# Kernel optimization log

Measured on AMD Instinct MI355X. Metric: run time of the kernel, lower is better.

Reference implementation:

```python
import jax, jax.numpy as jnp
import numpy as np

BATCH, NODES, CH_IN, CH_OUT, N_EXPERTS = 8, 8192, 128, 128, 64

def setup_inputs() -> dict:
    key = jax.random.key(0)
    kx, kw, ks = jax.random.split(key, 3)
    x = jax.random.normal(kx, (BATCH, NODES, CH_IN), dtype=jnp.float32)
    # std = fan_in**-0.5 per self_init
    W = jax.random.normal(kw, (N_EXPERTS, CH_OUT, CH_IN), dtype=jnp.float32) * (CH_IN ** -0.5)
    sel = jax.random.randint(ks, (NODES,), 0, N_EXPERTS, dtype=jnp.int64)
    return {"x": x, "sel": sel, "W": W}

def reference(x, sel, W):
    # x: (b, n, j), W[sel]: (n, i, j) -> out: (b, n, i)
    Wsel = W[sel]  # gather a (ch_out, ch_in) matrix per node
    return jnp.einsum('bnj,nij->bni', x, Wsel)
```

## Files before the change

### kernel.cpp

```cpp
#include <hip/hip_runtime.h>

#define BATCH   8
#define NODES   8192
#define CH      128
#define NEXP    64
#define TN      16
#define MAXP    (NODES + NEXP * TN)
#define NTILES  (MAXP / TN)

typedef __attribute__((ext_vector_type(8))) short bf16x8;
typedef __attribute__((ext_vector_type(4))) float f32x4;

__device__ __forceinline__ bf16x8 cvt8(f32x4 lo, f32x4 hi) {
    bf16x8 r;
    #pragma unroll
    for (int i = 0; i < 4; ++i) {
        r[i]     = (short)__builtin_bit_cast(unsigned short, static_cast<__bf16>(lo[i]));
        r[i + 4] = (short)__builtin_bit_cast(unsigned short, static_cast<__bf16>(hi[i]));
    }
    return r;
}

__global__ __launch_bounds__(256)
void prep_kernel(const int* __restrict__ sel, const float* __restrict__ W,
                 short* __restrict__ Wbf, int* __restrict__ sorted)
{
    const int t = threadIdx.x;

    {
        const size_t base = (size_t)blockIdx.x * (CH * CH / 4);
        const float* ws = W   + base;
        short*       wd = Wbf + base;
        #pragma unroll
        for (int i = 0; i < 2; ++i) {
            int idx = (i * 256 + t) * 8;
            f32x4 lo = *reinterpret_cast<const f32x4*>(ws + idx);
            f32x4 hi = *reinterpret_cast<const f32x4*>(ws + idx + 4);
            *reinterpret_cast<bf16x8*>(wd + idx) = cvt8(lo, hi);
        }
    }

    const int e = blockIdx.x;
    if (e >= NEXP) return;

    const int wv = t >> 6;
    __shared__ int wcnt[4][NEXP];
    __shared__ int s_off, s_cnt, s_total, cursor;
    if (t < NEXP) { wcnt[0][t] = 0; wcnt[1][t] = 0; wcnt[2][t] = 0; wcnt[3][t] = 0; }
    if (t == 0) cursor = 0;
    __syncthreads();

    int myv[NODES / 256];
    #pragma unroll
    for (int i = 0; i < NODES / 256; ++i) {
        myv[i] = sel[i * 256 + t];
        atomicAdd(&wcnt[wv][myv[i]], 1);
    }
    __syncthreads();

    if (t < NEXP) {
        int c = wcnt[0][t] + wcnt[1][t] + wcnt[2][t] + wcnt[3][t];
        int p = (c + TN - 1) & ~(TN - 1);
        int scan = p;
        #pragma unroll
        for (int d = 1; d < NEXP; d <<= 1) {
            int v = __shfl_up(scan, d);
            if (t >= d) scan += v;
        }
        if (t == e)        { s_off = scan - p; s_cnt = c; }
        if (t == NEXP - 1) s_total = scan;
    }
    __syncthreads();

    const int off = s_off, myc = s_cnt;
    const int pad = (myc + TN - 1) & ~(TN - 1);

    for (int i = myc + t; i < pad; i += 256) sorted[off + i] = -1;

    if (e == NEXP - 1) {
        for (int i = s_total + t; i < MAXP; i += 256) sorted[i] = -1;
    }

    #pragma unroll
    for (int i = 0; i < NODES / 256; ++i) {
        if (myv[i] == e) {
            int pos = atomicAdd(&cursor, 1);
            sorted[off + pos] = i * 256 + t;
        }
    }
}

__global__ __launch_bounds__(512)
void gemm_kernel(const float* __restrict__ x, const int* __restrict__ sel,
                 const short* __restrict__ Wbf, float* __restrict__ out,
                 const int* __restrict__ sorted)
{
    __shared__ int s_nodes[TN];
    __shared__ int s_expert;

    const int tid  = threadIdx.x;
    const int tile = blockIdx.x;

    if (tid < TN) s_nodes[tid] = sorted[tile * TN + tid];
    if (tid == 0) {
        int n0 = sorted[tile * TN];
        s_expert = (n0 >= 0) ? sel[n0] : -1;
    }
    __syncthreads();

    const int e = s_expert;
    if (e < 0) return;

    const int wave = tid >> 6;
    const int lane = tid & 63;
    const int m16  = lane & 15;
    const int quad = lane >> 4;

    const int r    = wave * 16 + m16;
    const int node = s_nodes[r >> 3];
    const int b    = r & 7;
    const int nd   = (node >= 0) ? node : 0;
    const float* xrow  = x + ((size_t)(b * NODES + nd)) * CH;
    const short* wbase = Wbf + (size_t)e * CH * CH;

    f32x4 acc[8];
    #pragma unroll
    for (int ct = 0; ct < 8; ++ct) acc[ct] = (f32x4){0.f, 0.f, 0.f, 0.f};

    #pragma unroll
    for (int kk = 0; kk < 4; ++kk) {
        const int k0 = kk * 32 + quad * 8;

        f32x4 lo = *reinterpret_cast<const f32x4*>(xrow + k0);
        f32x4 hi = *reinterpret_cast<const f32x4*>(xrow + k0 + 4);
        bf16x8 afrag = cvt8(lo, hi);

        #pragma unroll
        for (int ct = 0; ct < 8; ++ct) {
            bf16x8 bfrag = *reinterpret_cast<const bf16x8*>(
                wbase + (size_t)(ct * 16 + m16) * CH + k0);
            acc[ct] = __builtin_amdgcn_mfma_f32_16x16x32_bf16(
                          afrag, bfrag, acc[ct], 0, 0, 0);
        }
    }

    #pragma unroll
    for (int reg = 0; reg < 4; ++reg) {
        int rr = wave * 16 + quad * 4 + reg;
        int nn = s_nodes[rr >> 3];
        if (nn < 0) continue;
        int bb = rr & 7;
        float* orow = out + ((size_t)(bb * NODES + nn)) * CH;
        #pragma unroll
        for (int ct = 0; ct < 8; ++ct)
            orow[ct * 16 + m16] = acc[ct][reg];
    }
}

extern "C" void kernel_launch(void* const* d_in, const int* in_sizes, int n_in,
                              void* d_out, int out_size, void* d_ws, size_t ws_size,
                              hipStream_t stream)
{
    const float* x   = (const float*)d_in[0];
    const int*   sel = (const int*)  d_in[1];
    const float* W   = (const float*)d_in[2];
    float*       out = (float*)d_out;

    short* Wbf    = (short*)d_ws;
    int*   sorted = (int*)((char*)d_ws + (size_t)NEXP * CH * CH * sizeof(short));

    prep_kernel<<<256, 256, 0, stream>>>(sel, W, Wbf, sorted);
    gemm_kernel<<<NTILES, 512, 0, stream>>>(x, sel, Wbf, out, sorted);
}
```

Baseline: 124.3 us.

## Swap MFMA operands for vectorized stores and reuse W fragments across two row tiles

```diff
diff --git a/kernel.cpp b/kernel.cpp
--- a/kernel.cpp
+++ b/kernel.cpp
@@ -90,7 +90,7 @@
     }
 }
 
-__global__ __launch_bounds__(512)
+__global__ __launch_bounds__(256)
 void gemm_kernel(const float* __restrict__ x, const int* __restrict__ sel,
                  const short* __restrict__ Wbf, float* __restrict__ out,
                  const int* __restrict__ sorted)
@@ -116,44 +116,60 @@
     const int m16  = lane & 15;
     const int quad = lane >> 4;
 
-    const int r    = wave * 16 + m16;
-    const int node = s_nodes[r >> 3];
-    const int b    = r & 7;
-    const int nd   = (node >= 0) ? node : 0;
-    const float* xrow  = x + ((size_t)(b * NODES + nd)) * CH;
+    int          nodej[2];
+    const float* xrow[2];
+    #pragma unroll
+    for (int jt = 0; jt < 2; ++jt) {
+        int j    = wave * 32 + jt * 16 + m16;
+        int node = s_nodes[j >> 3];
+        int b    = j & 7;
+        nodej[jt] = node;
+        int nd   = (node >= 0) ? node : 0;
+        xrow[jt] = x + ((size_t)(b * NODES + nd)) * CH;
+    }
     const short* wbase = Wbf + (size_t)e * CH * CH;
 
-    f32x4 acc[8];
+    f32x4 acc[2][8];
     #pragma unroll
-    for (int ct = 0; ct < 8; ++ct) acc[ct] = (f32x4){0.f, 0.f, 0.f, 0.f};
+    for (int jt = 0; jt < 2; ++jt)
+        #pragma unroll
+        for (int ct = 0; ct < 8; ++ct)
+            acc[jt][ct] = (f32x4){0.f, 0.f, 0.f, 0.f};
 
     #pragma unroll
     for (int kk = 0; kk < 4; ++kk) {
         const int k0 = kk * 32 + quad * 8;
 
-        f32x4 lo = *reinterpret_cast<const f32x4*>(xrow + k0);
-        f32x4 hi = *reinterpret_cast<const f32x4*>(xrow + k0 + 4);
-        bf16x8 afrag = cvt8(lo, hi);
+        bf16x8 xfrag[2];
+        #pragma unroll
+        for (int jt = 0; jt < 2; ++jt) {
+            const float* p = xrow[jt] + k0;
+            f32x4 lo = *reinterpret_cast<const f32x4*>(p);
+            f32x4 hi = *reinterpret_cast<const f32x4*>(p + 4);
+            xfrag[jt] = cvt8(lo, hi);
+        }
 
         #pragma unroll
         for (int ct = 0; ct < 8; ++ct) {
-            bf16x8 bfrag = *reinterpret_cast<const bf16x8*>(
+            bf16x8 wfrag = *reinterpret_cast<const bf16x8*>(
                 wbase + (size_t)(ct * 16 + m16) * CH + k0);
-            acc[ct] = __builtin_amdgcn_mfma_f32_16x16x32_bf16(
-                          afrag, bfrag, acc[ct], 0, 0, 0);
+            acc[0][ct] = __builtin_amdgcn_mfma_f32_16x16x32_bf16(
+                             wfrag, xfrag[0], acc[0][ct], 0, 0, 0);
+            acc[1][ct] = __builtin_amdgcn_mfma_f32_16x16x32_bf16(
+                             wfrag, xfrag[1], acc[1][ct], 0, 0, 0);
         }
     }
 
     #pragma unroll
-    for (int reg = 0; reg < 4; ++reg) {
-        int rr = wave * 16 + quad * 4 + reg;
-        int nn = s_nodes[rr >> 3];
-        if (nn < 0) continue;
-        int bb = rr & 7;
-        float* orow = out + ((size_t)(bb * NODES + nn)) * CH;
+    for (int jt = 0; jt < 2; ++jt) {
+        int node = nodej[jt];
+        if (node < 0) continue;
+        int j = wave * 32 + jt * 16 + m16;
+        int b = j & 7;
+        float* orow = out + ((size_t)(b * NODES + node)) * CH;
         #pragma unroll
         for (int ct = 0; ct < 8; ++ct)
-            orow[ct * 16 + m16] = acc[ct][reg];
+            *reinterpret_cast<f32x4*>(orow + ct * 16 + quad * 4) = acc[jt][ct];
     }
 }
 
@@ -170,5 +186,5 @@
     int*   sorted = (int*)((char*)d_ws + (size_t)NEXP * CH * CH * sizeof(short));
 
     prep_kernel<<<256, 256, 0, stream>>>(sel, W, Wbf, sorted);
-    gemm_kernel<<<NTILES, 512, 0, stream>>>(x, sel, Wbf, out, sorted);
+    gemm_kernel<<<NTILES, 256, 0, stream>>>(x, sel, Wbf, out, sorted);
 }
```

Measured after the change: 116.8 us. 6.1% less time.
